# Performance work log

Measured on AMD Instinct MI355X. Metric: run time of the kernel, lower is better.

The kernel has to match this reference:

```python
import jax, jax.numpy as jnp
import numpy as np

HEADS = 16
DIM_HEAD = 64
SCALE = DIM_HEAD ** -0.5
NEG = -jnp.finfo(jnp.float32).max


def setup_inputs() -> dict:
    key = jax.random.key(0)
    k1, k2, k3, k4, k5 = jax.random.split(key, 5)
    dim = 1024
    inner = HEADS * DIM_HEAD
    b, n = 2, 2048
    s = dim ** -0.5
    return {
        "x": jax.random.normal(k1, (b, n, dim), dtype=jnp.float32),
        "Wq": jax.random.normal(k2, (dim, inner), dtype=jnp.float32) * s,
        "Wk": jax.random.normal(k3, (dim, inner), dtype=jnp.float32) * s,
        "Wv": jax.random.normal(k4, (dim, inner), dtype=jnp.float32) * s,
        "Wo": jax.random.normal(k5, (inner, dim), dtype=jnp.float32) * s,
    }


def reference(x, Wq, Wk, Wv, Wo):
    b, n, _ = x.shape
    # project and split heads: b n (h d) -> b h n d
    def split(t):
        return t.reshape(b, n, HEADS, DIM_HEAD).transpose(0, 2, 1, 3)
    q = split(x @ Wq) * SCALE
    k = split(x @ Wk)
    v = split(x @ Wv)
    sim = jnp.einsum('bhid,bhjd->bhij', q, k)
    # causal mask: triu(j - i + 1) masked with -finfo.max
    causal = jnp.triu(jnp.ones((n, n), dtype=bool), k=1)
    sim = jnp.where(causal, NEG, sim)
    attn = jax.nn.softmax(sim, axis=-1)  # dropout p=0.0 -> identity
    out = jnp.einsum('bhij,bhjd->bhid', attn, v)
    out = out.transpose(0, 2, 1, 3).reshape(b, n, HEADS * DIM_HEAD)
    return out @ Wo
```

## Files before the change

kernel.cpp:

```cpp
#include <hip/hip_runtime.h>

#define NHEAD 16
#define DHEAD 64
#define SEQ 2048
#define DMODEL 1024
#define BATCH 2
#define QSCALE 0.1803368801111204f

typedef __bf16 bf16x8 __attribute__((ext_vector_type(8)));
typedef float f32x4 __attribute__((ext_vector_type(4)));
typedef float f32x16 __attribute__((ext_vector_type(16)));
typedef unsigned int u32x4 __attribute__((ext_vector_type(4)));

__device__ inline unsigned short f2bf(float f) {
  unsigned int u = __builtin_bit_cast(unsigned int, f);
  u = (u + 0x7FFFu + ((u >> 16) & 1u)) >> 16;
  return (unsigned short)u;
}

__device__ inline unsigned int cvtpk_bf16(float lo, float hi) {
  unsigned int r;
  asm("v_cvt_pk_bf16_f32 %0, %1, %2" : "=v"(r) : "v"(lo), "v"(hi));
  return r;
}

__device__ inline void pl32swap(unsigned int& a, unsigned int& b) {
  asm volatile("v_permlane32_swap_b32 %0, %1" : "+v"(a), "+v"(b));
}

typedef __attribute__((address_space(1))) unsigned int GU32;
typedef __attribute__((address_space(3))) unsigned int LU32;
__device__ inline void gld_lds16(const void* g, void* l) {
  __builtin_amdgcn_global_load_lds((GU32*)g, (LU32*)l, 16, 0, 0);
}

__global__ __launch_bounds__(256) void k_conv_x(const float* __restrict__ x,
                                                unsigned short* __restrict__ xb) {
  int i = blockIdx.x * 256 + threadIdx.x;
  float4 v = ((const float4*)x)[i];
  ushort4 o;
  o.x = f2bf(v.x); o.y = f2bf(v.y); o.z = f2bf(v.z); o.w = f2bf(v.w);
  ((ushort4*)xb)[i] = o;
}

__global__ __launch_bounds__(256) void k_trans_w(const float* __restrict__ Wq, const float* __restrict__ Wk,
                                                 const float* __restrict__ Wv, const float* __restrict__ Wo,
                                                 unsigned short* __restrict__ Wqt, unsigned short* __restrict__ Wkt,
                                                 unsigned short* __restrict__ Wvt, unsigned short* __restrict__ Wot) {
  __shared__ float ts[64][65];
  int z = blockIdx.z;
  const float* src = (z == 0) ? Wq : (z == 1) ? Wk : (z == 2) ? Wv : Wo;
  unsigned short* dst = (z == 0) ? Wqt : (z == 1) ? Wkt : (z == 2) ? Wvt : Wot;
  int r0 = blockIdx.y * 64, c0 = blockIdx.x * 64;
  int t = threadIdx.x;
  int tr = t >> 4, tc = (t & 15) * 4;
#pragma unroll
  for (int i = 0; i < 4; i++) {
    int row = tr + i * 16;
    float4 v = *(const float4*)&src[(size_t)(r0 + row) * DMODEL + c0 + tc];
    ts[row][tc + 0] = v.x; ts[row][tc + 1] = v.y; ts[row][tc + 2] = v.z; ts[row][tc + 3] = v.w;
  }
  __syncthreads();
#pragma unroll
  for (int i = 0; i < 4; i++) {
    int nrow = tr + i * 16;
    ushort4 o;
    o.x = f2bf(ts[tc + 0][nrow]); o.y = f2bf(ts[tc + 1][nrow]);
    o.z = f2bf(ts[tc + 2][nrow]); o.w = f2bf(ts[tc + 3][nrow]);
    *(ushort4*)&dst[(size_t)(c0 + nrow) * DMODEL + r0 + tc] = o;
  }
}

__device__ inline void gemm_core(const unsigned short* __restrict__ A, const unsigned short* __restrict__ Bt,
                                 int brow0, int bcol0, unsigned short* As, unsigned short* Bs,
                                 f32x4 acc[4][4]) {
  int tid = threadIdx.x, lane = tid & 63, wave = tid >> 6;
  int wr = wave >> 1, wc = wave & 1;
  for (int kt = 0; kt < DMODEL / 32; ++kt) {
    int k0 = kt * 32;
    if (kt) __syncthreads();
#pragma unroll
    for (int qi = 0; qi < 2; ++qi) {
      int e0 = (wave * 2 + qi) * 512;
      int e = e0 + lane * 8;
      gld_lds16(&A[(size_t)(brow0 + (e >> 5)) * DMODEL + k0 + (e & 31)], &As[e0]);
      gld_lds16(&Bt[(size_t)(bcol0 + (e >> 5)) * DMODEL + k0 + (e & 31)], &Bs[e0]);
    }
    __syncthreads();
    bf16x8 af[4], bff[4];
#pragma unroll
    for (int i = 0; i < 4; i++)
      af[i] = *(const bf16x8*)&As[(wr * 64 + i * 16 + (lane & 15)) * 32 + (lane >> 4) * 8];
#pragma unroll
    for (int j = 0; j < 4; j++)
      bff[j] = *(const bf16x8*)&Bs[(wc * 64 + j * 16 + (lane & 15)) * 32 + (lane >> 4) * 8];
#pragma unroll
    for (int i = 0; i < 4; i++)
#pragma unroll
      for (int j = 0; j < 4; j++)
        acc[i][j] = __builtin_amdgcn_mfma_f32_16x16x32_bf16(af[i], bff[j], acc[i][j], 0, 0, 0);
  }
}

__global__ __launch_bounds__(256) void k_gemm_qkv(const unsigned short* __restrict__ xb,
                                                  const unsigned short* __restrict__ Wqt,
                                                  const unsigned short* __restrict__ Wkt,
                                                  const unsigned short* __restrict__ Wvt,
                                                  unsigned short* __restrict__ Qf,
                                                  unsigned short* __restrict__ Kf,
                                                  unsigned short* __restrict__ Vf) {
  __shared__ unsigned short As[128 * 32];
  __shared__ unsigned short Bs[128 * 32];
  int bx = blockIdx.x;
  int wsel = bx >> 3;
  int col0 = (bx & 7) * 128;
  int brow0 = blockIdx.y * 128;
  const unsigned short* Bt = (wsel == 0) ? Wqt : (wsel == 1) ? Wkt : Wvt;
  int lane = threadIdx.x & 63, wave = threadIdx.x >> 6;
  int wr = wave >> 1, wc = wave & 1;
  f32x4 acc[4][4] = {};
  gemm_core(xb, Bt, brow0, col0, As, Bs, acc);
#pragma unroll
  for (int i = 0; i < 4; i++)
#pragma unroll
    for (int j = 0; j < 4; j++) {
      int n_g = brow0 + wr * 64 + i * 16 + ((lane >> 4) << 2);
      int c = col0 + wc * 64 + j * 16 + (lane & 15);
      int b = n_g >> 11, n0 = n_g & 2047;
      int h = c >> 6, d = c & 63;
      int bh = b * NHEAD + h;
      if (wsel == 0) {
        size_t base = ((size_t)(bh * 64 + (n0 >> 5)) * 4 + (d >> 4)) * 512 +
                      (size_t)((((d >> 3) & 1) * 32 + (n0 & 31)) * 8 + (d & 7));
#pragma unroll
        for (int r = 0; r < 4; r++) Qf[base + 8 * r] = f2bf(acc[i][j][r] * QSCALE);
      } else if (wsel == 1) {
        size_t base = ((size_t)(bh * 32 + (n0 >> 6)) * 8 + ((d >> 4) + 4 * ((n0 >> 5) & 1))) * 512 +
                      (size_t)((((d >> 3) & 1) * 32 + (n0 & 31)) * 8 + (d & 7));
#pragma unroll
        for (int r = 0; r < 4; r++) Kf[base + 8 * r] = f2bf(acc[i][j][r]);
      } else {
        size_t base = ((size_t)(bh * 32 + (n0 >> 6)) * 8 + (((n0 >> 4) & 3) + 4 * (d >> 5))) * 512 +
                      (size_t)((((n0 >> 3) & 1) * 32 + (d & 31)) * 8 + (n0 & 7));
        ushort4 o;
        o.x = f2bf(acc[i][j][0]); o.y = f2bf(acc[i][j][1]);
        o.z = f2bf(acc[i][j][2]); o.w = f2bf(acc[i][j][3]);
        *(ushort4*)&Vf[base] = o;
      }
    }
}

__global__ __launch_bounds__(64, 2) void k_attn(const unsigned short* __restrict__ Qf,
                                                const unsigned short* __restrict__ Kf,
                                                const unsigned short* __restrict__ Vf,
                                                unsigned short* __restrict__ Ob) {
  int id = blockIdx.x;
  int xcd = id & 7, m = id >> 3;
  int bhl = m & 3, u = m >> 2;
  int bh = xcd * 4 + bhl;
  int v = (u < 32) ? (63 - u) : (u - 32);
  int nk = (v >> 1) + 1;
  int lane = threadIdx.x;
  int h = lane >> 5, ql = lane & 31;
  int qrow = v * 32 + ql;

  const unsigned short* Qp = Qf + (size_t)bh * 131072 + (size_t)v * 2048;
  const unsigned short* Kp = Kf + (size_t)bh * 131072;
  const unsigned short* Vp = Vf + (size_t)bh * 131072;
  int b = bh >> 4, hh = bh & 15;

  bf16x8 qv[4];
#pragma unroll
  for (int ds = 0; ds < 4; ds++)
    qv[ds] = *(const bf16x8*)&Qp[ds * 512 + lane * 8];

  bf16x8 Kr[8], Vr[8];
#pragma unroll
  for (int jj = 0; jj < 8; jj++) Kr[jj] = *(const bf16x8*)&Kp[jj * 512 + lane * 8];
#pragma unroll
  for (int jj = 0; jj < 8; jj++) Vr[jj] = *(const bf16x8*)&Vp[jj * 512 + lane * 8];

  f32x16 o0 = {}, o1 = {};
  float m_r = -3.0e38f, l_r = 0.0f;

#pragma unroll 1
  for (int kc = 0; kc < nk; ++kc) {
    f32x16 s0 = {}, s1 = {};
#pragma unroll
    for (int ds = 0; ds < 4; ds++) {
      s0 = __builtin_amdgcn_mfma_f32_32x32x16_bf16(Kr[ds], qv[ds], s0, 0, 0, 0);
      s1 = __builtin_amdgcn_mfma_f32_32x32x16_bf16(Kr[4 + ds], qv[ds], s1, 0, 0, 0);
    }
    bool pfn = (kc + 1 < nk);
    size_t nb = (size_t)(kc + 1) * 4096;
    if (pfn) {
#pragma unroll
      for (int jj = 0; jj < 8; jj++) Kr[jj] = *(const bf16x8*)&Kp[nb + jj * 512 + lane * 8];
    }
    int k0 = kc * 64;
    if (kc == nk - 1) {
#pragma unroll
      for (int r = 0; r < 16; r++) {
        int kloc = (r & 3) + 8 * (r >> 2) + 4 * h;
        if (k0 + kloc > qrow) s0[r] = -3.0e38f;
        if (k0 + 32 + kloc > qrow) s1[r] = -3.0e38f;
      }
    }
    float t0[8], t1[8];
#pragma unroll
    for (int r = 0; r < 8; r++) t0[r] = fmaxf(s0[r], s0[r + 8]);
#pragma unroll
    for (int r = 0; r < 8; r++) t1[r] = fmaxf(s1[r], s1[r + 8]);
#pragma unroll
    for (int r = 0; r < 4; r++) t0[r] = fmaxf(fmaxf(t0[r], t0[r + 4]), fmaxf(t1[r], t1[r + 4]));
    float pm = fmaxf(fmaxf(t0[0], t0[1]), fmaxf(t0[2], t0[3]));
    pm = fmaxf(pm, __shfl_xor(pm, 32));
    bool grow = pm > m_r + 8.0f;
    float mnew = grow ? pm : m_r;
    float sf = grow ? __builtin_amdgcn_exp2f(m_r - mnew) : 1.0f;
    m_r = mnew;
    float rsum = 0.0f;
#pragma unroll
    for (int r = 0; r < 16; r++) { s0[r] = __builtin_amdgcn_exp2f(s0[r] - m_r); rsum += s0[r]; }
#pragma unroll
    for (int r = 0; r < 16; r++) { s1[r] = __builtin_amdgcn_exp2f(s1[r] - m_r); rsum += s1[r]; }
    l_r = l_r * sf + rsum;
    if (__ballot(grow)) {
#pragma unroll
      for (int r = 0; r < 16; r++) { o0[r] *= sf; o1[r] *= sf; }
    }
    unsigned int pa0 = cvtpk_bf16(s0[0], s0[1]),   pa1 = cvtpk_bf16(s0[2], s0[3]);
    unsigned int pb0 = cvtpk_bf16(s0[4], s0[5]),   pb1 = cvtpk_bf16(s0[6], s0[7]);
    unsigned int pc0 = cvtpk_bf16(s0[8], s0[9]),   pc1 = cvtpk_bf16(s0[10], s0[11]);
    unsigned int pd0 = cvtpk_bf16(s0[12], s0[13]), pd1 = cvtpk_bf16(s0[14], s0[15]);
    unsigned int pe0 = cvtpk_bf16(s1[0], s1[1]),   pe1 = cvtpk_bf16(s1[2], s1[3]);
    unsigned int pf0 = cvtpk_bf16(s1[4], s1[5]),   pf1 = cvtpk_bf16(s1[6], s1[7]);
    unsigned int pg0 = cvtpk_bf16(s1[8], s1[9]),   pg1 = cvtpk_bf16(s1[10], s1[11]);
    unsigned int ph0 = cvtpk_bf16(s1[12], s1[13]), ph1 = cvtpk_bf16(s1[14], s1[15]);
    pl32swap(pa0, pb0); pl32swap(pa1, pb1);
    pl32swap(pc0, pd0); pl32swap(pc1, pd1);
    pl32swap(pe0, pf0); pl32swap(pe1, pf1);
    pl32swap(pg0, ph0); pl32swap(pg1, ph1);
    bf16x8 pfr[4];
    pfr[0] = __builtin_bit_cast(bf16x8, (u32x4){pa0, pa1, pb0, pb1});
    pfr[1] = __builtin_bit_cast(bf16x8, (u32x4){pc0, pc1, pd0, pd1});
    pfr[2] = __builtin_bit_cast(bf16x8, (u32x4){pe0, pe1, pf0, pf1});
    pfr[3] = __builtin_bit_cast(bf16x8, (u32x4){pg0, pg1, ph0, ph1});
#pragma unroll
    for (int ks = 0; ks < 4; ks++) {
      o0 = __builtin_amdgcn_mfma_f32_32x32x16_bf16(Vr[ks], pfr[ks], o0, 0, 0, 0);
      o1 = __builtin_amdgcn_mfma_f32_32x32x16_bf16(Vr[4 + ks], pfr[ks], o1, 0, 0, 0);
    }
    if (pfn) {
#pragma unroll
      for (int jj = 0; jj < 8; jj++) Vr[jj] = *(const bf16x8*)&Vp[nb + jj * 512 + lane * 8];
    }
  }

  float lt = l_r + __shfl_xor(l_r, 32);
  float rl = 1.0f / lt;
  size_t obase = ((size_t)(b * SEQ + qrow)) * DMODEL + hh * DHEAD;
#pragma unroll
  for (int rg = 0; rg < 4; rg++) {
    uint2 w0, w1;
    w0.x = cvtpk_bf16(o0[4 * rg] * rl, o0[4 * rg + 1] * rl);
    w0.y = cvtpk_bf16(o0[4 * rg + 2] * rl, o0[4 * rg + 3] * rl);
    w1.x = cvtpk_bf16(o1[4 * rg] * rl, o1[4 * rg + 1] * rl);
    w1.y = cvtpk_bf16(o1[4 * rg + 2] * rl, o1[4 * rg + 3] * rl);
    *(uint2*)&Ob[obase + 8 * rg + 4 * h] = w0;
    *(uint2*)&Ob[obase + 32 + 8 * rg + 4 * h] = w1;
  }
}

__global__ __launch_bounds__(256) void k_gemm_out(const unsigned short* __restrict__ Ob,
                                                  const unsigned short* __restrict__ Wot,
                                                  float* __restrict__ out) {
  __shared__ unsigned short As[128 * 32];
  __shared__ unsigned short Bs[128 * 32];
  int col0 = blockIdx.x * 128;
  int brow0 = blockIdx.y * 128;
  int lane = threadIdx.x & 63, wave = threadIdx.x >> 6;
  int wr = wave >> 1, wc = wave & 1;
  f32x4 acc[4][4] = {};
  gemm_core(Ob, Wot, brow0, col0, As, Bs, acc);
#pragma unroll
  for (int i = 0; i < 4; i++)
#pragma unroll
    for (int j = 0; j < 4; j++)
#pragma unroll
      for (int r = 0; r < 4; r++) {
        int row = brow0 + wr * 64 + i * 16 + ((lane >> 4) << 2) + r;
        int c = col0 + wc * 64 + j * 16 + (lane & 15);
        out[(size_t)row * DMODEL + c] = acc[i][j][r];
      }
}

extern "C" void kernel_launch(void* const* d_in, const int* in_sizes, int n_in,
                              void* d_out, int out_size, void* d_ws, size_t ws_size,
                              hipStream_t stream) {
  const float* x  = (const float*)d_in[0];
  const float* Wq = (const float*)d_in[1];
  const float* Wk = (const float*)d_in[2];
  const float* Wv = (const float*)d_in[3];
  const float* Wo = (const float*)d_in[4];
  float* out = (float*)d_out;
  char* ws = (char*)d_ws;
  unsigned short* xb  = (unsigned short*)(ws);
  unsigned short* Wqt = (unsigned short*)(ws + (8ull << 20));
  unsigned short* Wkt = (unsigned short*)(ws + (10ull << 20));
  unsigned short* Wvt = (unsigned short*)(ws + (12ull << 20));
  unsigned short* Wot = (unsigned short*)(ws + (14ull << 20));
  unsigned short* Qf  = (unsigned short*)(ws + (16ull << 20));
  unsigned short* Kf  = (unsigned short*)(ws + (24ull << 20));
  unsigned short* Vf  = (unsigned short*)(ws + (32ull << 20));
  unsigned short* Ob  = (unsigned short*)(ws + (40ull << 20));

  k_conv_x<<<dim3(4096), dim3(256), 0, stream>>>(x, xb);
  k_trans_w<<<dim3(16, 16, 4), dim3(256), 0, stream>>>(Wq, Wk, Wv, Wo, Wqt, Wkt, Wvt, Wot);
  k_gemm_qkv<<<dim3(24, 32), dim3(256), 0, stream>>>(xb, Wqt, Wkt, Wvt, Qf, Kf, Vf);
  k_attn<<<dim3(2048), dim3(64), 0, stream>>>(Qf, Kf, Vf, Ob);
  k_gemm_out<<<dim3(8, 32), dim3(256), 0, stream>>>(Ob, Wot, out);
}
```

Baseline: 124.2 us.

## Pre-swizzle x and QKV weights into MFMA fragment layout, LDS-free QKV GEMM

The x conversion and Wq/Wk/Wv transposes now write bf16 data directly in the per-lane MFMA fragment order, so the QKV GEMM can load operands straight from global memory into registers without LDS staging or barriers. The QKV GEMM becomes single-wave 64x64 tiles with register double-buffering, and blocks are mapped so each XCD shares weight column groups for L2 reuse. Wo keeps the old transpose kernel. In exchange there is less data reuse per block (64x64 tiles instead of 128x128) and more global/L2 traffic, and global-load latency is hidden only by the two-deep register prefetch.

```diff
diff --git a/kernel.cpp b/kernel.cpp
--- a/kernel.cpp
+++ b/kernel.cpp
@@ -35,29 +35,66 @@
 }
 
 __global__ __launch_bounds__(256) void k_conv_x(const float* __restrict__ x,
-                                                unsigned short* __restrict__ xb) {
-  int i = blockIdx.x * 256 + threadIdx.x;
-  float4 v = ((const float4*)x)[i];
-  ushort4 o;
-  o.x = f2bf(v.x); o.y = f2bf(v.y); o.z = f2bf(v.z); o.w = f2bf(v.w);
-  ((ushort4*)xb)[i] = o;
-}
-
-__global__ __launch_bounds__(256) void k_trans_w(const float* __restrict__ Wq, const float* __restrict__ Wk,
-                                                 const float* __restrict__ Wv, const float* __restrict__ Wo,
-                                                 unsigned short* __restrict__ Wqt, unsigned short* __restrict__ Wkt,
-                                                 unsigned short* __restrict__ Wvt, unsigned short* __restrict__ Wot) {
+                                                unsigned short* __restrict__ Af) {
+  int blk = blockIdx.x;
+  int R = blk >> 5, kt = blk & 31;
+  int t = threadIdx.x;
+  int i = t >> 6, lane = t & 63;
+  int n = R * 64 + i * 16 + (lane & 15);
+  int k = kt * 32 + (lane >> 4) * 8;
+  const float* xp = x + (size_t)n * DMODEL + k;
+  float4 v0 = *(const float4*)xp;
+  float4 v1 = *(const float4*)(xp + 4);
+  ushort4 lo, hi;
+  lo.x = f2bf(v0.x); lo.y = f2bf(v0.y); lo.z = f2bf(v0.z); lo.w = f2bf(v0.w);
+  hi.x = f2bf(v1.x); hi.y = f2bf(v1.y); hi.z = f2bf(v1.z); hi.w = f2bf(v1.w);
+  size_t base = ((size_t)((R * 32 + kt) * 4 + i) * 64 + lane) * 8;
+  *(ushort4*)&Af[base] = lo;
+  *(ushort4*)&Af[base + 4] = hi;
+}
+
+__global__ __launch_bounds__(256) void k_trans_wf(const float* __restrict__ Wq, const float* __restrict__ Wk,
+                                                  const float* __restrict__ Wv,
+                                                  unsigned short* __restrict__ Wqf, unsigned short* __restrict__ Wkf,
+                                                  unsigned short* __restrict__ Wvf) {
+  __shared__ float ts[32][65];
+  int mat = blockIdx.z;
+  const float* src = (mat == 0) ? Wq : (mat == 1) ? Wk : Wv;
+  unsigned short* dst = (mat == 0) ? Wqf : (mat == 1) ? Wkf : Wvf;
+  int cb = blockIdx.x, kt = blockIdx.y;
+  int t = threadIdx.x;
+  int row = t >> 3, seg = t & 7;
+  const float* sp = src + (size_t)(kt * 32 + row) * DMODEL + cb * 64 + seg * 8;
+  float4 u0 = *(const float4*)sp;
+  float4 u1 = *(const float4*)(sp + 4);
+  ts[row][seg * 8 + 0] = u0.x; ts[row][seg * 8 + 1] = u0.y;
+  ts[row][seg * 8 + 2] = u0.z; ts[row][seg * 8 + 3] = u0.w;
+  ts[row][seg * 8 + 4] = u1.x; ts[row][seg * 8 + 5] = u1.y;
+  ts[row][seg * 8 + 6] = u1.z; ts[row][seg * 8 + 7] = u1.w;
+  __syncthreads();
+  int j = t >> 6, lane = t & 63;
+  int c_l = j * 16 + (lane & 15);
+  int kb = (lane >> 4) * 8;
+  ushort4 lo, hi;
+  lo.x = f2bf(ts[kb + 0][c_l]); lo.y = f2bf(ts[kb + 1][c_l]);
+  lo.z = f2bf(ts[kb + 2][c_l]); lo.w = f2bf(ts[kb + 3][c_l]);
+  hi.x = f2bf(ts[kb + 4][c_l]); hi.y = f2bf(ts[kb + 5][c_l]);
+  hi.z = f2bf(ts[kb + 6][c_l]); hi.w = f2bf(ts[kb + 7][c_l]);
+  size_t base = ((size_t)((cb * 32 + kt) * 4 + j) * 64 + lane) * 8;
+  *(ushort4*)&dst[base] = lo;
+  *(ushort4*)&dst[base + 4] = hi;
+}
+
+__global__ __launch_bounds__(256) void k_trans_wo(const float* __restrict__ Wo,
+                                                  unsigned short* __restrict__ Wot) {
   __shared__ float ts[64][65];
-  int z = blockIdx.z;
-  const float* src = (z == 0) ? Wq : (z == 1) ? Wk : (z == 2) ? Wv : Wo;
-  unsigned short* dst = (z == 0) ? Wqt : (z == 1) ? Wkt : (z == 2) ? Wvt : Wot;
   int r0 = blockIdx.y * 64, c0 = blockIdx.x * 64;
   int t = threadIdx.x;
   int tr = t >> 4, tc = (t & 15) * 4;
 #pragma unroll
   for (int i = 0; i < 4; i++) {
     int row = tr + i * 16;
-    float4 v = *(const float4*)&src[(size_t)(r0 + row) * DMODEL + c0 + tc];
+    float4 v = *(const float4*)&Wo[(size_t)(r0 + row) * DMODEL + c0 + tc];
     ts[row][tc + 0] = v.x; ts[row][tc + 1] = v.y; ts[row][tc + 2] = v.z; ts[row][tc + 3] = v.w;
   }
   __syncthreads();
@@ -67,74 +104,83 @@
     ushort4 o;
     o.x = f2bf(ts[tc + 0][nrow]); o.y = f2bf(ts[tc + 1][nrow]);
     o.z = f2bf(ts[tc + 2][nrow]); o.w = f2bf(ts[tc + 3][nrow]);
-    *(ushort4*)&dst[(size_t)(c0 + nrow) * DMODEL + r0 + tc] = o;
-  }
-}
-
-__device__ inline void gemm_core(const unsigned short* __restrict__ A, const unsigned short* __restrict__ Bt,
-                                 int brow0, int bcol0, unsigned short* As, unsigned short* Bs,
-                                 f32x4 acc[4][4]) {
-  int tid = threadIdx.x, lane = tid & 63, wave = tid >> 6;
-  int wr = wave >> 1, wc = wave & 1;
-  for (int kt = 0; kt < DMODEL / 32; ++kt) {
-    int k0 = kt * 32;
-    if (kt) __syncthreads();
-#pragma unroll
-    for (int qi = 0; qi < 2; ++qi) {
-      int e0 = (wave * 2 + qi) * 512;
-      int e = e0 + lane * 8;
-      gld_lds16(&A[(size_t)(brow0 + (e >> 5)) * DMODEL + k0 + (e & 31)], &As[e0]);
-      gld_lds16(&Bt[(size_t)(bcol0 + (e >> 5)) * DMODEL + k0 + (e & 31)], &Bs[e0]);
-    }
-    __syncthreads();
-    bf16x8 af[4], bff[4];
+    *(ushort4*)&Wot[(size_t)(c0 + nrow) * DMODEL + r0 + tc] = o;
+  }
+}
+
+__global__ __launch_bounds__(64, 2) void k_gemm_qkv(const unsigned short* __restrict__ Af,
+                                                    const unsigned short* __restrict__ Wqf,
+                                                    const unsigned short* __restrict__ Wkf,
+                                                    const unsigned short* __restrict__ Wvf,
+                                                    unsigned short* __restrict__ Qf,
+                                                    unsigned short* __restrict__ Kf,
+                                                    unsigned short* __restrict__ Vf) {
+  int id = blockIdx.x;
+  int xcd = id & 7, lid = id >> 3;
+  int rg = lid / 96, rem = lid - rg * 96;
+  int cq = rem >> 4, rr = rem & 15;
+  int R = rg * 16 + rr;
+  int Cg = xcd * 6 + cq;
+  int mat = Cg >> 4, cb = Cg & 15;
+  const unsigned short* Bf = (mat == 0) ? Wqf : (mat == 1) ? Wkf : Wvf;
+  int lane = threadIdx.x;
+  const unsigned short* Ap = Af + (size_t)R * 65536 + lane * 8;
+  const unsigned short* Bp = Bf + (size_t)cb * 65536 + lane * 8;
+
+  f32x4 acc[4][4] = {};
+  bf16x8 a0[4], b0[4], a1[4], b1[4];
+#pragma unroll
+  for (int i = 0; i < 4; i++) {
+    a0[i] = *(const bf16x8*)(Ap + i * 512);
+    b0[i] = *(const bf16x8*)(Bp + i * 512);
+  }
+#pragma unroll 1
+  for (int kt = 0; kt < 32; kt += 2) {
+    {
+      const unsigned short* An = Ap + (kt + 1) * 2048;
+      const unsigned short* Bn = Bp + (kt + 1) * 2048;
+#pragma unroll
+      for (int i = 0; i < 4; i++) {
+        a1[i] = *(const bf16x8*)(An + i * 512);
+        b1[i] = *(const bf16x8*)(Bn + i * 512);
+      }
+    }
 #pragma unroll
     for (int i = 0; i < 4; i++)
-      af[i] = *(const bf16x8*)&As[(wr * 64 + i * 16 + (lane & 15)) * 32 + (lane >> 4) * 8];
-#pragma unroll
-    for (int j = 0; j < 4; j++)
-      bff[j] = *(const bf16x8*)&Bs[(wc * 64 + j * 16 + (lane & 15)) * 32 + (lane >> 4) * 8];
+#pragma unroll
+      for (int j = 0; j < 4; j++)
+        acc[i][j] = __builtin_amdgcn_mfma_f32_16x16x32_bf16(a0[i], b0[j], acc[i][j], 0, 0, 0);
+    if (kt + 2 < 32) {
+      const unsigned short* An = Ap + (kt + 2) * 2048;
+      const unsigned short* Bn = Bp + (kt + 2) * 2048;
+#pragma unroll
+      for (int i = 0; i < 4; i++) {
+        a0[i] = *(const bf16x8*)(An + i * 512);
+        b0[i] = *(const bf16x8*)(Bn + i * 512);
+      }
+    }
 #pragma unroll
     for (int i = 0; i < 4; i++)
 #pragma unroll
       for (int j = 0; j < 4; j++)
-        acc[i][j] = __builtin_amdgcn_mfma_f32_16x16x32_bf16(af[i], bff[j], acc[i][j], 0, 0, 0);
-  }
-}
-
-__global__ __launch_bounds__(256) void k_gemm_qkv(const unsigned short* __restrict__ xb,
-                                                  const unsigned short* __restrict__ Wqt,
-                                                  const unsigned short* __restrict__ Wkt,
-                                                  const unsigned short* __restrict__ Wvt,
-                                                  unsigned short* __restrict__ Qf,
-                                                  unsigned short* __restrict__ Kf,
-                                                  unsigned short* __restrict__ Vf) {
-  __shared__ unsigned short As[128 * 32];
-  __shared__ unsigned short Bs[128 * 32];
-  int bx = blockIdx.x;
-  int wsel = bx >> 3;
-  int col0 = (bx & 7) * 128;
-  int brow0 = blockIdx.y * 128;
-  const unsigned short* Bt = (wsel == 0) ? Wqt : (wsel == 1) ? Wkt : Wvt;
-  int lane = threadIdx.x & 63, wave = threadIdx.x >> 6;
-  int wr = wave >> 1, wc = wave & 1;
-  f32x4 acc[4][4] = {};
-  gemm_core(xb, Bt, brow0, col0, As, Bs, acc);
+        acc[i][j] = __builtin_amdgcn_mfma_f32_16x16x32_bf16(a1[i], b1[j], acc[i][j], 0, 0, 0);
+  }
+
 #pragma unroll
   for (int i = 0; i < 4; i++)
 #pragma unroll
     for (int j = 0; j < 4; j++) {
-      int n_g = brow0 + wr * 64 + i * 16 + ((lane >> 4) << 2);
-      int c = col0 + wc * 64 + j * 16 + (lane & 15);
+      int n_g = R * 64 + i * 16 + ((lane >> 4) << 2);
+      int c = cb * 64 + j * 16 + (lane & 15);
       int b = n_g >> 11, n0 = n_g & 2047;
       int h = c >> 6, d = c & 63;
       int bh = b * NHEAD + h;
-      if (wsel == 0) {
+      if (mat == 0) {
         size_t base = ((size_t)(bh * 64 + (n0 >> 5)) * 4 + (d >> 4)) * 512 +
                       (size_t)((((d >> 3) & 1) * 32 + (n0 & 31)) * 8 + (d & 7));
 #pragma unroll
         for (int r = 0; r < 4; r++) Qf[base + 8 * r] = f2bf(acc[i][j][r] * QSCALE);
-      } else if (wsel == 1) {
+      } else if (mat == 1) {
         size_t base = ((size_t)(bh * 32 + (n0 >> 6)) * 8 + ((d >> 4) + 4 * ((n0 >> 5) & 1))) * 512 +
                       (size_t)((((d >> 3) & 1) * 32 + (n0 & 31)) * 8 + (d & 7));
 #pragma unroll
@@ -148,6 +194,37 @@
         *(ushort4*)&Vf[base] = o;
       }
     }
+}
+
+__device__ inline void gemm_core(const unsigned short* __restrict__ A, const unsigned short* __restrict__ Bt,
+                                 int brow0, int bcol0, unsigned short* As, unsigned short* Bs,
+                                 f32x4 acc[4][4]) {
+  int tid = threadIdx.x, lane = tid & 63, wave = tid >> 6;
+  int wr = wave >> 1, wc = wave & 1;
+  for (int kt = 0; kt < DMODEL / 32; ++kt) {
+    int k0 = kt * 32;
+    if (kt) __syncthreads();
+#pragma unroll
+    for (int qi = 0; qi < 2; ++qi) {
+      int e0 = (wave * 2 + qi) * 512;
+      int e = e0 + lane * 8;
+      gld_lds16(&A[(size_t)(brow0 + (e >> 5)) * DMODEL + k0 + (e & 31)], &As[e0]);
+      gld_lds16(&Bt[(size_t)(bcol0 + (e >> 5)) * DMODEL + k0 + (e & 31)], &Bs[e0]);
+    }
+    __syncthreads();
+    bf16x8 af[4], bff[4];
+#pragma unroll
+    for (int i = 0; i < 4; i++)
+      af[i] = *(const bf16x8*)&As[(wr * 64 + i * 16 + (lane & 15)) * 32 + (lane >> 4) * 8];
+#pragma unroll
+    for (int j = 0; j < 4; j++)
+      bff[j] = *(const bf16x8*)&Bs[(wc * 64 + j * 16 + (lane & 15)) * 32 + (lane >> 4) * 8];
+#pragma unroll
+    for (int i = 0; i < 4; i++)
+#pragma unroll
+      for (int j = 0; j < 4; j++)
+        acc[i][j] = __builtin_amdgcn_mfma_f32_16x16x32_bf16(af[i], bff[j], acc[i][j], 0, 0, 0);
+  }
 }
 
 __global__ __launch_bounds__(64, 2) void k_attn(const unsigned short* __restrict__ Qf,
@@ -305,19 +382,20 @@
   const float* Wo = (const float*)d_in[4];
   float* out = (float*)d_out;
   char* ws = (char*)d_ws;
-  unsigned short* xb  = (unsigned short*)(ws);
-  unsigned short* Wqt = (unsigned short*)(ws + (8ull << 20));
-  unsigned short* Wkt = (unsigned short*)(ws + (10ull << 20));
-  unsigned short* Wvt = (unsigned short*)(ws + (12ull << 20));
+  unsigned short* Af  = (unsigned short*)(ws);
+  unsigned short* Wqf = (unsigned short*)(ws + (8ull << 20));
+  unsigned short* Wkf = (unsigned short*)(ws + (10ull << 20));
+  unsigned short* Wvf = (unsigned short*)(ws + (12ull << 20));
   unsigned short* Wot = (unsigned short*)(ws + (14ull << 20));
   unsigned short* Qf  = (unsigned short*)(ws + (16ull << 20));
   unsigned short* Kf  = (unsigned short*)(ws + (24ull << 20));
   unsigned short* Vf  = (unsigned short*)(ws + (32ull << 20));
   unsigned short* Ob  = (unsigned short*)(ws + (40ull << 20));
 
-  k_conv_x<<<dim3(4096), dim3(256), 0, stream>>>(x, xb);
-  k_trans_w<<<dim3(16, 16, 4), dim3(256), 0, stream>>>(Wq, Wk, Wv, Wo, Wqt, Wkt, Wvt, Wot);
-  k_gemm_qkv<<<dim3(24, 32), dim3(256), 0, stream>>>(xb, Wqt, Wkt, Wvt, Qf, Kf, Vf);
+  k_conv_x<<<dim3(2048), dim3(256), 0, stream>>>(x, Af);
+  k_trans_wf<<<dim3(16, 32, 3), dim3(256), 0, stream>>>(Wq, Wk, Wv, Wqf, Wkf, Wvf);
+  k_trans_wo<<<dim3(16, 16), dim3(256), 0, stream>>>(Wo, Wot);
+  k_gemm_qkv<<<dim3(3072), dim3(64), 0, stream>>>(Af, Wqf, Wkf, Wvf, Qf, Kf, Vf);
   k_attn<<<dim3(2048), dim3(64), 0, stream>>>(Qf, Kf, Vf, Ob);
   k_gemm_out<<<dim3(8, 32), dim3(256), 0, stream>>>(Ob, Wot, out);
 }
```

New measurement: 112.1 us. 1.11x faster.
